# Kernel optimization log

Measured on AMD Instinct MI355X. Metric: run time of the kernel, lower is better.

Reference implementation:

```python
import jax, jax.numpy as jnp
import numpy as np

B, H, E = 8192, 1024, 8


def setup_inputs() -> dict:
    key = jax.random.key(0)
    ks = jax.random.split(key, 6)
    scale = 0.02  # keep gate/expert logits in a sane range
    return {
        "x": jax.random.normal(ks[0], (B, H), jnp.float32),
        "class_label": jax.random.randint(ks[1], (B,), 0, 2),
        "gate_w": jax.random.normal(ks[2], (E, H), jnp.float32) * scale,
        "w1": jax.random.normal(ks[3], (E, H, H), jnp.float32) * scale,
        "b1": jnp.zeros((E, H), jnp.float32),
        "w2": jax.random.normal(ks[4], (E, H, 2), jnp.float32) * scale,
        "b2": jnp.zeros((E, 2), jnp.float32),
    }


def reference(x, class_label, gate_w, w1, b1, w2, b2):
    num_experts = w1.shape[0]
    # --- router ---
    logits = x @ gate_w.T                              # [B, E]
    routing_prob = jax.nn.softmax(logits, axis=-1)     # [B, E]
    idx = jnp.argmax(routing_prob, axis=-1)            # [B] top-1 expert
    dispatch_onehot = jax.nn.one_hot(idx, num_experts, dtype=jnp.float32)
    balancing_loss = (routing_prob.mean(axis=0) * dispatch_onehot.mean(axis=0)).sum() * num_experts
    router_z_loss = jnp.mean(jax.nn.logsumexp(logits, axis=-1) ** 2)
    # --- experts: compute all experts densely, then select the routed one ---
    h = jax.nn.gelu(jnp.einsum('bh,ehd->bed', x, w1) + b1[None], approximate=False)  # [B, E, H]
    probs = jax.nn.softmax(jnp.einsum('bed,edc->bec', h, w2) + b2[None], axis=-1)    # [B, E, 2]
    expert_out = jnp.take_along_axis(probs, idx[:, None, None], axis=1)[:, 0, :]     # [B, 2]
    # --- straight-through-style weight: value 1, grad flows through p_max ---
    p_max = routing_prob.max(axis=-1)                  # [B]
    weight = p_max + jax.lax.stop_gradient(1.0 - p_max)
    weighted_logits = expert_out * weight[:, None]     # [B, 2]
    # CrossEntropyLoss applied on (already softmaxed) outputs, faithful to source
    logp = jax.nn.log_softmax(weighted_logits, axis=-1)
    ce_loss = -jnp.take_along_axis(logp, class_label[:, None], axis=1).mean()
    loss = ce_loss + 0.01 * balancing_loss + 0.001 * router_z_loss
    return loss
```

## Files before the change

### kernel.cpp

```cpp
#include <hip/hip_runtime.h>
#include <math.h>

#define BQ 8192
#define HD 1024
#define NE 8
#define CAP 1280

#define BM 128
#define BN 128
#define BK 64
#define NRT 10
#define NCT 8
#define TILES_PER_E 80


#define WS_CURSOR   0
#define WS_S        64
#define WS_ZSUM     96
#define WS_CESUM    100
#define WS_ROWLIST  128
#define WS_LOGITS2  41088
#define WS_XC       123008
#define WS_W1T      10608768

using f32x4  = __attribute__((ext_vector_type(4))) float;

__device__ __forceinline__ float gelu_exact(float v) {
    return 0.5f * v * (1.0f + erff(v * 0.70710678118654752440f));
}

__device__ __forceinline__ unsigned int f4_to_fp8x4(float f0, float f1, float f2, float f3) {
    int lo = __builtin_amdgcn_cvt_pk_fp8_f32(f0, f1, 0, false);
    return (unsigned int)__builtin_amdgcn_cvt_pk_fp8_f32(f2, f3, lo, true);
}

__device__ __forceinline__ void gll16(const void* g, void* l) {
    __builtin_amdgcn_global_load_lds((const __attribute__((address_space(1))) void*)g,
                                     (__attribute__((address_space(3))) void*)l, 16, 0, 0);
}

__global__ __launch_bounds__(256) void zero_kernel(float4* __restrict__ logits2c4,
                                                   int* __restrict__ head)
{
    int t = blockIdx.x * 256 + threadIdx.x;
    if (blockIdx.x == 0 && threadIdx.x < 32) head[threadIdx.x] = 0;
    if (t < NE * CAP * 2 / 4)
        logits2c4[t] = make_float4(0.f, 0.f, 0.f, 0.f);
}

__global__ __launch_bounds__(256) void prep_kernel(
    const float* __restrict__ x, const float* __restrict__ gate_w,
    const float* __restrict__ w1,
    int* __restrict__ cursor, float* __restrict__ S, float* __restrict__ zsum,
    int* __restrict__ rowlist, unsigned char* __restrict__ xcq,
    unsigned char* __restrict__ w1tq)
{
    __shared__ __align__(16) char smem[33280];
    int tid = threadIdx.x;

    if (blockIdx.x >= 256) {
        char (*lt)[80] = (char (*)[80])smem;
        int tile = blockIdx.x - 256;
        int e = tile >> 8;
        int rem = tile & 255;
        int k0 = (rem >> 4) << 6, n0 = (rem & 15) << 6;
        const float* src = w1 + ((size_t)e << 20) + (size_t)k0 * HD + n0;
        #pragma unroll
        for (int s = 0; s < 4; s++) {
            int q = tid + s * 256;
            int kk = q >> 4, n4 = q & 15;
            float4 v = *(const float4*)(src + (size_t)kk * HD + n4 * 4);
            unsigned int b = f4_to_fp8x4(v.x * 8.f, v.y * 8.f, v.z * 8.f, v.w * 8.f);
            lt[n4 * 4 + 0][kk] = (char)(b);
            lt[n4 * 4 + 1][kk] = (char)(b >> 8);
            lt[n4 * 4 + 2][kk] = (char)(b >> 16);
            lt[n4 * 4 + 3][kk] = (char)(b >> 24);
        }
        __syncthreads();
        int nn = tid >> 2, q = tid & 3;
        int pos0 = ((q & 1) << 5) | ((q >> 1) << 3);
        unsigned char* dst = w1tq + ((size_t)e << 20) + (size_t)(n0 + nn) * HD + k0;
        const unsigned long long* sp = (const unsigned long long*)&lt[nn][q * 16];
        *(unsigned long long*)(dst + pos0)      = sp[0];
        *(unsigned long long*)(dst + pos0 + 16) = sp[1];
        return;
    }

    float* gw    = (float*)smem;
    float* sS    = (float*)(smem + 32768);
    float* sZ    = (float*)(smem + 32800);
    int*   sBI   = (int*)(smem + 32832);
    int*   sSlot = (int*)(smem + 32960);
    int*   sBase = (int*)(smem + 33088);

    for (int i = tid * 4; i < NE * HD; i += 256 * 4) {
        *(float4*)(gw + i) = *(const float4*)(gate_w + i);
    }
    if (tid < NE) sS[tid] = 0.f;
    if (tid == 0) sZ[0] = 0.f;
    __syncthreads();

    int wave = tid >> 6, lane = tid & 63;
    int r0 = blockIdx.x * 32;
    float accS[NE];
    #pragma unroll
    for (int e = 0; e < NE; e++) accS[e] = 0.f;
    float accZ = 0.f;

    #pragma unroll 1
    for (int i = 0; i < 8; i++) {
        int li = wave * 8 + i;
        int r = r0 + li;
        const float* xr = x + (size_t)r * HD;
        float acc[NE];
        #pragma unroll
        for (int e = 0; e < NE; e++) acc[e] = 0.f;
        #pragma unroll
        for (int it = 0; it < 4; it++) {
            int k = lane * 4 + it * 256;
            float4 xv = *(const float4*)(xr + k);
            #pragma unroll
            for (int e = 0; e < NE; e++) {
                const float* g = gw + e * HD + k;
                acc[e] += xv.x * g[0] + xv.y * g[1] + xv.z * g[2] + xv.w * g[3];
            }
        }
        #pragma unroll
        for (int e = 0; e < NE; e++) {
            #pragma unroll
            for (int off = 32; off > 0; off >>= 1)
                acc[e] += __shfl_xor(acc[e], off);
        }
        if (lane == 0) {
            float m = acc[0]; int bi = 0;
            #pragma unroll
            for (int e = 1; e < NE; e++) if (acc[e] > m) { m = acc[e]; bi = e; }
            float se = 0.f, ex[NE];
            #pragma unroll
            for (int e = 0; e < NE; e++) { ex[e] = expf(acc[e] - m); se += ex[e]; }
            float inv = 1.f / se;
            #pragma unroll
            for (int e = 0; e < NE; e++) accS[e] += ex[e] * inv;
            float lse = m + logf(se);
            accZ += lse * lse;
            sBI[li] = bi;
        }
    }
    if (lane == 0) {
        #pragma unroll
        for (int e = 0; e < NE; e++) atomicAdd(&sS[e], accS[e]);
        atomicAdd(sZ, accZ);
    }
    __syncthreads();

    if (tid < NE) {
        int cnt = 0;
        #pragma unroll
        for (int j = 0; j < 32; j++) cnt += (sBI[j] == tid);
        sBase[tid] = atomicAdd(&cursor[tid], cnt);
        atomicAdd(&S[tid], sS[tid]);
    }
    if (tid == 0) atomicAdd(zsum, sZ[0]);
    __syncthreads();

    if (tid < 32) {
        int bi = sBI[tid];
        int rank = 0;
        for (int j = 0; j < tid; j++) rank += (sBI[j] == bi);
        int slot = sBase[bi] + rank;
        sSlot[tid] = slot;
        if (slot < CAP) rowlist[bi * CAP + slot] = r0 + tid;
    }
    __syncthreads();

    #pragma unroll 1
    for (int i = 0; i < 8; i++) {
        int li = wave * 8 + i;
        int bi = sBI[li];
        int pos = sSlot[li];
        if (pos >= CAP) continue;
        const float* src = x + (size_t)(r0 + li) * HD + lane * 16;
        float4 v0 = *(const float4*)(src + 0);
        float4 v1 = *(const float4*)(src + 4);
        float4 v2 = *(const float4*)(src + 8);
        float4 v3 = *(const float4*)(src + 12);
        unsigned int g0a = f4_to_fp8x4(v0.x, v0.y, v0.z, v0.w);
        unsigned int g0b = f4_to_fp8x4(v1.x, v1.y, v1.z, v1.w);
        unsigned int g1a = f4_to_fp8x4(v2.x, v2.y, v2.z, v2.w);
        unsigned int g1b = f4_to_fp8x4(v3.x, v3.y, v3.z, v3.w);
        int s = lane >> 2, q = lane & 3;
        int pos0 = (s << 6) | ((q & 1) << 5) | ((q >> 1) << 3);
        unsigned char* dst = xcq + ((size_t)(bi * CAP + pos)) * HD;
        *(unsigned long long*)(dst + pos0)      = (unsigned long long)g0a | ((unsigned long long)g0b << 32);
        *(unsigned long long*)(dst + pos0 + 16) = (unsigned long long)g1a | ((unsigned long long)g1b << 32);
    }
}

__global__ __launch_bounds__(256, 3) void expert_gemm_kernel(
    const unsigned char* __restrict__ xcq, const unsigned char* __restrict__ w1tq,
    const float* __restrict__ b1, const float* __restrict__ w2,
    const int* __restrict__ cursor, float* __restrict__ logits2c)
{
    int bid = blockIdx.x;
    int e = bid & 7;
    int tix = bid >> 3;
    int col = tix / NRT;
    int rt = tix - col * NRT;
    int cnt = cursor[e]; if (cnt > CAP) cnt = CAP;
    if (rt * BM >= cnt) return;
    int n0 = col * BN;

    __shared__ __align__(16) char lds[3][16384];

    int t = threadIdx.x;
    int l = t & 63;
    int scolb = ((t & 3) ^ ((t >> 3) & 3)) << 4;
    int m = t >> 2;

    int wid = t >> 6;
    int wr = wid >> 1, wc = wid & 1;
    int r = l & 15, h = l >> 4;
    int off = (h << 4) ^ (((r >> 1) & 3) << 4);

    const unsigned char* xcp  = xcq + ((size_t)e * CAP) * HD;
    const unsigned char* w1tp = w1tq + ((size_t)e << 20);

    const unsigned char* srcA0 = xcp + (size_t)(rt * BM + m) * HD + scolb;
    const unsigned char* srcA1 = srcA0 + (size_t)64 * HD;
    const unsigned char* srcB0 = w1tp + (size_t)(n0 + m) * HD + scolb;
    const unsigned char* srcB1 = srcB0 + (size_t)64 * HD;

    f32x4 acc[4][4];
    #pragma unroll
    for (int i = 0; i < 4; i++)
        #pragma unroll
        for (int j = 0; j < 4; j++) acc[i][j] = (f32x4)(0.f);

    auto stage = [&](int bi) {
        gll16(srcA0, lds[bi] + t * 16);         srcA0 += BK;
        gll16(srcA1, lds[bi] + 4096 + t * 16);  srcA1 += BK;
        gll16(srcB0, lds[bi] + 8192 + t * 16);  srcB0 += BK;
        gll16(srcB1, lds[bi] + 12288 + t * 16); srcB1 += BK;
    };
    auto compute = [&](int bi) {
        const char* Ar = lds[bi] + (wr * 64 + r) * 64 + off;
        const char* Br = lds[bi] + 8192 + (wc * 64 + r) * 64 + off;
        longlong2 av[4], bv[4];
        #pragma unroll
        for (int i = 0; i < 4; i++) {
            av[i] = *(const longlong2*)(Ar + i * 1024);
            bv[i] = *(const longlong2*)(Br + i * 1024);
        }
        #pragma unroll
        for (int i = 0; i < 4; i++)
            #pragma unroll
            for (int j = 0; j < 4; j++)
                acc[i][j] = __builtin_amdgcn_mfma_f32_16x16x32_fp8_fp8(av[i].x, bv[j].x, acc[i][j], 0, 0, 0);
        #pragma unroll
        for (int i = 0; i < 4; i++)
            #pragma unroll
            for (int j = 0; j < 4; j++)
                acc[i][j] = __builtin_amdgcn_mfma_f32_16x16x32_fp8_fp8(av[i].y, bv[j].y, acc[i][j], 0, 0, 0);
    };

    stage(0); stage(1);
    int cs = 2, cc = 0;
    #pragma unroll 1
    for (int it = 0; it < HD / BK - 2; ++it) {
        asm volatile("s_waitcnt vmcnt(4)" ::: "memory");
        __builtin_amdgcn_s_barrier();
        stage(cs); cs = (cs == 2) ? 0 : cs + 1;
        compute(cc); cc = (cc == 2) ? 0 : cc + 1;
    }
    asm volatile("s_waitcnt vmcnt(4)" ::: "memory");
    __builtin_amdgcn_s_barrier();
    compute(cc); cc = (cc == 2) ? 0 : cc + 1;
    asm volatile("s_waitcnt vmcnt(0)" ::: "memory");
    __builtin_amdgcn_s_barrier();
    compute(cc);

    float b1v[4], w20v[4], w21v[4];
    #pragma unroll
    for (int j = 0; j < 4; j++) {
        int cj = n0 + wc * 64 + j * 16 + r;
        b1v[j]  = b1[e * HD + cj];
        w20v[j] = w2[((size_t)e * HD + cj) * 2 + 0];
        w21v[j] = w2[((size_t)e * HD + cj) * 2 + 1];
    }
    #pragma unroll
    for (int i = 0; i < 4; i++) {
        #pragma unroll
        for (int reg = 0; reg < 4; reg++) {
            float s0 = 0.f, s1 = 0.f;
            #pragma unroll
            for (int j = 0; j < 4; j++) {
                float hv = gelu_exact(acc[i][j][reg] * 0.125f + b1v[j]);
                s0 += hv * w20v[j];
                s1 += hv * w21v[j];
            }
            #pragma unroll
            for (int offx = 1; offx < 16; offx <<= 1) {
                s0 += __shfl_xor(s0, offx);
                s1 += __shfl_xor(s1, offx);
            }
            if (r == 0) {
                int p = rt * BM + wr * 64 + i * 16 + 4 * h + reg;
                if (p < cnt) {
                    atomicAdd(&logits2c[(e * CAP + p) * 2 + 0], s0);
                    atomicAdd(&logits2c[(e * CAP + p) * 2 + 1], s1);
                }
            }
        }
    }
}

__global__ __launch_bounds__(256) void ce_kernel(
    const float* __restrict__ logits2c, const float* __restrict__ b2,
    const int* __restrict__ cursor, const int* __restrict__ rowlist,
    const int* __restrict__ label, float* __restrict__ cesum)
{
    __shared__ float red[4];
    int tid = threadIdx.x;
    int s = blockIdx.x * 256 + tid;
    int e = s / CAP;
    int local = s - e * CAP;
    int cnt = cursor[e]; if (cnt > CAP) cnt = CAP;
    float ce = 0.f;
    if (local < cnt) {
        int rr = rowlist[s];
        float l0 = logits2c[s * 2 + 0] + b2[e * 2 + 0];
        float l1 = logits2c[s * 2 + 1] + b2[e * 2 + 1];
        float mx = fmaxf(l0, l1);
        float e0 = expf(l0 - mx), e1 = expf(l1 - mx);
        float inv = 1.f / (e0 + e1);
        float p0 = e0 * inv, p1 = e1 * inv;
        float m2 = fmaxf(p0, p1);
        float z = m2 + logf(expf(p0 - m2) + expf(p1 - m2));
        float lp = ((label[rr] == 0) ? p0 : p1) - z;
        ce = -lp;
    }
    int lane = tid & 63, wave = tid >> 6;
    #pragma unroll
    for (int off = 32; off > 0; off >>= 1) ce += __shfl_xor(ce, off);
    if (lane == 0) red[wave] = ce;
    __syncthreads();
    if (tid == 0) atomicAdd(cesum, red[0] + red[1] + red[2] + red[3]);
}

__global__ void finalize_kernel(const float* __restrict__ S, const int* __restrict__ cursor,
                                const float* __restrict__ zsum, const float* __restrict__ cesum,
                                float* __restrict__ out)
{
    if (threadIdx.x == 0 && blockIdx.x == 0) {
        float bal = 0.f;
        for (int e = 0; e < NE; e++) bal += S[e] * (float)cursor[e];
        bal *= (float)NE / ((float)BQ * (float)BQ);
        out[0] = cesum[0] / (float)BQ + 0.01f * bal + 0.001f * (zsum[0] / (float)BQ);
    }
}

extern "C" void kernel_launch(void* const* d_in, const int* in_sizes, int n_in,
                              void* d_out, int out_size, void* d_ws, size_t ws_size,
                              hipStream_t stream) {
    const float* x      = (const float*)d_in[0];
    const int*   label  = (const int*)d_in[1];
    const float* gate_w = (const float*)d_in[2];
    const float* w1     = (const float*)d_in[3];
    const float* b1     = (const float*)d_in[4];
    const float* w2     = (const float*)d_in[5];
    const float* b2     = (const float*)d_in[6];
    float* out = (float*)d_out;

    char* ws = (char*)d_ws;
    int*   cursor   = (int*)(ws + WS_CURSOR);
    float* S        = (float*)(ws + WS_S);
    float* zsum     = (float*)(ws + WS_ZSUM);
    float* cesum    = (float*)(ws + WS_CESUM);
    int*   rowlist  = (int*)(ws + WS_ROWLIST);
    float* logits2c = (float*)(ws + WS_LOGITS2);
    unsigned char* xcq  = (unsigned char*)(ws + WS_XC);
    unsigned char* w1tq = (unsigned char*)(ws + WS_W1T);

    zero_kernel<<<(NE * CAP * 2 / 4 + 255) / 256, 256, 0, stream>>>(
        (float4*)logits2c, (int*)ws);
    prep_kernel<<<2304, 256, 0, stream>>>(x, gate_w, w1, cursor, S, zsum,
                                          rowlist, xcq, w1tq);
    expert_gemm_kernel<<<NE * TILES_PER_E, 256, 0, stream>>>(xcq, w1tq, b1, w2,
                                                             cursor, logits2c);
    ce_kernel<<<NE * CAP / 256, 256, 0, stream>>>(logits2c, b2, cursor, rowlist,
                                                  label, cesum);
    finalize_kernel<<<1, 64, 0, stream>>>(S, cursor, zsum, cesum, out);
}
```

Baseline: 72.38 us.

## Fuse finalize into ce kernel with ticket and widen prep stores to 16B

Removes the separate finalize launch: the last CE block, found by an atomic ticket counter, computes the final loss after a threadfence. The fp8 packing stores for both x and the transposed w1 change from paired 8-byte writes to single 16-byte writes, with the source reads reordered so the K-interleaved layout is kept. The ticket relies on being zeroed by the existing zero kernel, which clears the workspace header, and it adds atomic reads in the final block.

```diff
diff --git a/kernel.cpp b/kernel.cpp
--- a/kernel.cpp
+++ b/kernel.cpp
@@ -18,6 +18,7 @@
 #define WS_S        64
 #define WS_ZSUM     96
 #define WS_CESUM    100
+#define WS_TICKET   104
 #define WS_ROWLIST  128
 #define WS_LOGITS2  41088
 #define WS_XC       123008
@@ -78,11 +79,12 @@
         }
         __syncthreads();
         int nn = tid >> 2, q = tid & 3;
-        int pos0 = ((q & 1) << 5) | ((q >> 1) << 3);
-        unsigned char* dst = w1tq + ((size_t)e << 20) + (size_t)(n0 + nn) * HD + k0;
-        const unsigned long long* sp = (const unsigned long long*)&lt[nn][q * 16];
-        *(unsigned long long*)(dst + pos0)      = sp[0];
-        *(unsigned long long*)(dst + pos0 + 16) = sp[1];
+        unsigned long long lo = *(const unsigned long long*)&lt[nn][8 * q];
+        unsigned long long hi = *(const unsigned long long*)&lt[nn][32 + 8 * q];
+        uint4 o;
+        o.x = (unsigned int)lo; o.y = (unsigned int)(lo >> 32);
+        o.z = (unsigned int)hi; o.w = (unsigned int)(hi >> 32);
+        *(uint4*)(w1tq + ((size_t)e << 20) + (size_t)(n0 + nn) * HD + k0 + q * 16) = o;
         return;
     }
 
@@ -179,20 +181,18 @@
         int bi = sBI[li];
         int pos = sSlot[li];
         if (pos >= CAP) continue;
-        const float* src = x + (size_t)(r0 + li) * HD + lane * 16;
-        float4 v0 = *(const float4*)(src + 0);
-        float4 v1 = *(const float4*)(src + 4);
-        float4 v2 = *(const float4*)(src + 8);
-        float4 v3 = *(const float4*)(src + 12);
-        unsigned int g0a = f4_to_fp8x4(v0.x, v0.y, v0.z, v0.w);
-        unsigned int g0b = f4_to_fp8x4(v1.x, v1.y, v1.z, v1.w);
-        unsigned int g1a = f4_to_fp8x4(v2.x, v2.y, v2.z, v2.w);
-        unsigned int g1b = f4_to_fp8x4(v3.x, v3.y, v3.z, v3.w);
-        int s = lane >> 2, q = lane & 3;
-        int pos0 = (s << 6) | ((q & 1) << 5) | ((q >> 1) << 3);
-        unsigned char* dst = xcq + ((size_t)(bi * CAP + pos)) * HD;
-        *(unsigned long long*)(dst + pos0)      = (unsigned long long)g0a | ((unsigned long long)g0b << 32);
-        *(unsigned long long*)(dst + pos0 + 16) = (unsigned long long)g1a | ((unsigned long long)g1b << 32);
+        int s = lane >> 2, c = lane & 3;
+        const float* src = x + (size_t)(r0 + li) * HD + (s << 6) + (c << 3);
+        float4 a0 = *(const float4*)(src);
+        float4 a1 = *(const float4*)(src + 4);
+        float4 h0 = *(const float4*)(src + 32);
+        float4 h1 = *(const float4*)(src + 36);
+        uint4 o;
+        o.x = f4_to_fp8x4(a0.x, a0.y, a0.z, a0.w);
+        o.y = f4_to_fp8x4(a1.x, a1.y, a1.z, a1.w);
+        o.z = f4_to_fp8x4(h0.x, h0.y, h0.z, h0.w);
+        o.w = f4_to_fp8x4(h1.x, h1.y, h1.z, h1.w);
+        *(uint4*)(xcq + ((size_t)(bi * CAP + pos)) * HD + (s << 6) + (c << 4)) = o;
     }
 }
 
@@ -316,8 +316,10 @@
 
 __global__ __launch_bounds__(256) void ce_kernel(
     const float* __restrict__ logits2c, const float* __restrict__ b2,
-    const int* __restrict__ cursor, const int* __restrict__ rowlist,
-    const int* __restrict__ label, float* __restrict__ cesum)
+    int* __restrict__ cursor, const int* __restrict__ rowlist,
+    const int* __restrict__ label, float* __restrict__ cesum,
+    float* __restrict__ S, float* __restrict__ zsum, int* __restrict__ ticket,
+    float* __restrict__ out)
 {
     __shared__ float red[4];
     int tid = threadIdx.x;
@@ -345,17 +347,23 @@
     if (lane == 0) red[wave] = ce;
     __syncthreads();
     if (tid == 0) atomicAdd(cesum, red[0] + red[1] + red[2] + red[3]);
-}
-
-__global__ void finalize_kernel(const float* __restrict__ S, const int* __restrict__ cursor,
-                                const float* __restrict__ zsum, const float* __restrict__ cesum,
-                                float* __restrict__ out)
-{
-    if (threadIdx.x == 0 && blockIdx.x == 0) {
-        float bal = 0.f;
-        for (int e = 0; e < NE; e++) bal += S[e] * (float)cursor[e];
-        bal *= (float)NE / ((float)BQ * (float)BQ);
-        out[0] = cesum[0] / (float)BQ + 0.01f * bal + 0.001f * (zsum[0] / (float)BQ);
+
+    __threadfence();
+    __syncthreads();
+    if (tid == 0) {
+        if (atomicAdd(ticket, 1) == (int)gridDim.x - 1) {
+            __threadfence();
+            float bal = 0.f;
+            for (int k = 0; k < NE; k++) {
+                float sk = atomicAdd(&S[k], 0.f);
+                int ck = atomicAdd(&cursor[k], 0);
+                bal += sk * (float)ck;
+            }
+            bal *= (float)NE / ((float)BQ * (float)BQ);
+            float cs = atomicAdd(cesum, 0.f);
+            float zs = atomicAdd(zsum, 0.f);
+            out[0] = cs / (float)BQ + 0.01f * bal + 0.001f * (zs / (float)BQ);
+        }
     }
 }
 
@@ -376,6 +384,7 @@
     float* S        = (float*)(ws + WS_S);
     float* zsum     = (float*)(ws + WS_ZSUM);
     float* cesum    = (float*)(ws + WS_CESUM);
+    int*   ticket   = (int*)(ws + WS_TICKET);
     int*   rowlist  = (int*)(ws + WS_ROWLIST);
     float* logits2c = (float*)(ws + WS_LOGITS2);
     unsigned char* xcq  = (unsigned char*)(ws + WS_XC);
@@ -388,6 +397,6 @@
     expert_gemm_kernel<<<NE * TILES_PER_E, 256, 0, stream>>>(xcq, w1tq, b1, w2,
                                                              cursor, logits2c);
     ce_kernel<<<NE * CAP / 256, 256, 0, stream>>>(logits2c, b2, cursor, rowlist,
-                                                  label, cesum);
-    finalize_kernel<<<1, 64, 0, stream>>>(S, cursor, zsum, cesum, out);
-}
+                                                  label, cesum, S, zsum, ticket,
+                                                  out);
+}
```

Measured after the change: 78.64 us. +8.7%, slower.
